# Kernel tuning notes

Measured on AMD Instinct MI355X. Metric: run time of the kernel, lower is better.

## Reference

```python
import jax, jax.numpy as jnp
import numpy as np

S, T, F, J, E, H = 1024, 64, 128, 64, 256, 4
DH = E // H


def layer_norm(x, g, b, eps=1e-10):
    m = jnp.mean(x, axis=-1, keepdims=True)
    v = jnp.mean((x - m) ** 2, axis=-1, keepdims=True)  # population var (correction=0)
    return (x - m) / jnp.sqrt(v + eps) * g + b


def mha(x, Wq, Wk, Wv):
    # x: [B, L, E]; Wq/Wk/Wv: [H, E, DH]. Non-standard: scale AFTER softmax@V.
    q = jnp.einsum('ble,hed->hbld', x, Wq)
    k = jnp.einsum('ble,hed->hbld', x, Wk)
    v = jnp.einsum('ble,hed->hbld', x, Wv)
    w = jax.nn.softmax(jnp.einsum('hbld,hbmd->hblm', q, k), axis=-1)
    o = jnp.einsum('hblm,hbmd->hbld', w, v) / jnp.sqrt(jnp.asarray(Wq.shape[-1], x.dtype))
    h, b, l, d = o.shape
    return jnp.transpose(o, (1, 2, 0, 3)).reshape(b, l, h * d)


def ffn(x, W1, b1, W2, b2):
    return jnp.maximum(x @ W1 + b1, 0.0) @ W2 + b2  # Dropout is identity in eval


def pos_encoding(t, e):
    pos = jnp.arange(t, dtype=jnp.float32)[:, None]
    two_i = jnp.floor(jnp.arange(e, dtype=jnp.float32) / 2.0) * 2.0
    div = jnp.power(jnp.float32(100004.0), two_i / e)
    pe = pos / div  # [t, e]
    pe = pe.at[:, 0::2].set(jnp.sin(pe[:, 0::2]))
    pe = pe.at[:, 1::2].set(jnp.cos(pe[:, 1::2]))
    return pe


def setup_inputs() -> dict:
    key = jax.random.key(0)
    ks = jax.random.split(key, 32)
    s = 0.02
    d = {}
    d['x'] = jax.random.normal(ks[0], (S, T, F + J), dtype=jnp.float32)
    d['gate_W'] = s * jax.random.normal(ks[1], (J, F))
    d['gate_b'] = s * jax.random.normal(ks[2], (F,))
    d['embed_W'] = s * jax.random.normal(ks[3], (F, E))
    d['ln0_g'] = 1.0 + s * jax.random.normal(ks[4], (E,))
    d['ln0_b'] = s * jax.random.normal(ks[5], (E,))
    d['intra_Wq'] = s * jax.random.normal(ks[6], (H, E, DH))
    d['intra_Wk'] = s * jax.random.normal(ks[7], (H, E, DH))
    d['intra_Wv'] = s * jax.random.normal(ks[8], (H, E, DH))
    d['intra_ln_g'] = 1.0 + s * jax.random.normal(ks[9], (E,))
    d['intra_ln_b'] = s * jax.random.normal(ks[10], (E,))
    d['intra_W1'] = s * jax.random.normal(ks[11], (E, 4 * E))
    d['intra_b1'] = s * jax.random.normal(ks[12], (4 * E,))
    d['intra_W2'] = s * jax.random.normal(ks[13], (4 * E, E))
    d['intra_b2'] = s * jax.random.normal(ks[14], (E,))
    d['inter_Wq'] = s * jax.random.normal(ks[15], (H, E, DH))
    d['inter_Wk'] = s * jax.random.normal(ks[16], (H, E, DH))
    d['inter_Wv'] = s * jax.random.normal(ks[17], (H, E, DH))
    d['inter_ln1_g'] = 1.0 + s * jax.random.normal(ks[18], (E,))
    d['inter_ln1_b'] = s * jax.random.normal(ks[19], (E,))
    d['inter_ln2_g'] = 1.0 + s * jax.random.normal(ks[20], (E,))
    d['inter_ln2_b'] = s * jax.random.normal(ks[21], (E,))
    d['inter_W1'] = s * jax.random.normal(ks[22], (E, 4 * E))
    d['inter_b1'] = s * jax.random.normal(ks[23], (4 * E,))
    d['inter_W2'] = s * jax.random.normal(ks[24], (4 * E, E))
    d['inter_b2'] = s * jax.random.normal(ks[25], (E,))
    d['temp_W'] = s * jax.random.normal(ks[26], (E, E))
    d['pred_W'] = s * jax.random.normal(ks[27], (E, 1))
    d['pred_b'] = s * jax.random.normal(ks[28], (1,))
    return d


def reference(x, gate_W, gate_b, embed_W, ln0_g, ln0_b,
              intra_Wq, intra_Wk, intra_Wv, intra_ln_g, intra_ln_b,
              intra_W1, intra_b1, intra_W2, intra_b2,
              inter_Wq, inter_Wk, inter_Wv, inter_ln1_g, inter_ln1_b,
              inter_ln2_g, inter_ln2_b, inter_W1, inter_b1, inter_W2, inter_b2,
              temp_W, pred_W, pred_b):
    # Gating
    x_f = x[..., :F]                       # [S, T, F]
    x_g = x[..., -1, F:]                   # [S, J]
    gate = jax.nn.softmax(x_g @ gate_W + gate_b, axis=-1)[:, None, :]
    x_f = gate * x_f
    # Embed + positional encoding + LN
    emb = x_f @ embed_W                    # [S, T, E]
    res = emb + pos_encoding(T, E)
    ln = layer_norm(res, ln0_g, ln0_b)
    # Intra-stock attention (attend over time axis per stock)
    a = mha(ln, intra_Wq, intra_Wk, intra_Wv)
    r = a + ln
    intra_out = r + ffn(layer_norm(r, intra_ln_g, intra_ln_b), intra_W1, intra_b1, intra_W2, intra_b2)
    # Inter-stock attention (attend over stock axis per timestep)
    xT = jnp.transpose(intra_out, (1, 0, 2))            # [T, S, E]
    xTn = layer_norm(xT, inter_ln1_g, inter_ln1_b)
    a2 = mha(xTn, inter_Wq, inter_Wk, inter_Wv)          # [T, S, E]
    out = jnp.transpose(a2, (1, 0, 2))                   # [S, T, E]
    r2 = out + intra_out
    inter_out = r2 + ffn(layer_norm(r2, inter_ln2_g, inter_ln2_b), inter_W1, inter_b1, inter_W2, inter_b2)
    # Temporal aggregation
    x1 = inter_out @ temp_W                              # [S, T, E]
    cur = x1[..., -1, :][..., :, None]                   # [S, E, 1]
    lam = jax.nn.softmax(jnp.squeeze(x1 @ cur, -1), axis=-1)[:, None, :]  # [S, 1, T]
    agg = jnp.squeeze(lam @ inter_out, -2)               # [S, E]
    # Prediction
    return agg @ pred_W + pred_b                         # [S, 1]
```

## Files before the change

kernel.cpp:

```cpp
#include <hip/hip_runtime.h>


typedef _Float16 h16;
typedef __attribute__((ext_vector_type(8))) _Float16 f16x8;
typedef __attribute__((ext_vector_type(4))) _Float16 f16x4;
typedef __attribute__((ext_vector_type(4))) float f32x4;

__device__ inline float wave_sum(float v){
  #pragma unroll
  for (int o=32;o;o>>=1) v += __shfl_xor(v,o);
  return v;
}
__device__ inline float wave_max(float v){
  #pragma unroll
  for (int o=32;o;o>>=1) v = fmaxf(v,__shfl_xor(v,o));
  return v;
}

__global__ __launch_bounds__(256) void k_pe(float* __restrict__ pe){
  int t = blockIdx.x, i = threadIdx.x;
  float two_i = (float)((i>>1)<<1);
  float dv = powf(100004.0f, two_i*(1.0f/256.0f));
  float v = (float)t / dv;
  pe[t*256+i] = (i&1) ? cosf(v) : sinf(v);
}

__global__ __launch_bounds__(64) void k_gate(const float* __restrict__ x,
    const float* __restrict__ gW, const float* __restrict__ gb,
    float* __restrict__ gate){
  int s = blockIdx.x, lane = threadIdx.x;
  __shared__ float xg[64];
  xg[lane] = x[((size_t)s*64+63)*192 + 128 + lane];
  __syncthreads();
  float a0 = gb[lane], a1 = gb[64+lane];
  #pragma unroll 4
  for (int j=0;j<64;j++){
    float xv = xg[j];
    a0 += xv*gW[j*128+lane];
    a1 += xv*gW[j*128+64+lane];
  }
  float mx = wave_max(fmaxf(a0,a1));
  float e0 = __expf(a0-mx), e1 = __expf(a1-mx);
  float sm = wave_sum(e0+e1);
  gate[s*128+lane]    = e0/sm;
  gate[s*128+64+lane] = e1/sm;
}

__global__ __launch_bounds__(256) void k_t16all(
    const float* __restrict__ q1, const float* __restrict__ k1, const float* __restrict__ v1,
    const float* __restrict__ q2, const float* __restrict__ k2, const float* __restrict__ v2,
    const float* __restrict__ embed_W, const float* __restrict__ temp_W,
    const float* __restrict__ iW1, const float* __restrict__ iW2,
    const float* __restrict__ eW1, const float* __restrict__ eW2,
    h16* __restrict__ base){
  __shared__ float tile[32][33];
  const int b = blockIdx.x, tid = threadIdx.x;
  const float* src; h16* dst; int K, N, tb; bool qkv = false;
  if (b < 384){
    int mat = b>>6; tb = b&63; qkv = true; K = 256; N = 256;
    src = (mat==0)?q1:(mat==1)?k1:(mat==2)?v1:(mat==3)?q2:(mat==4)?k2:v2;
    dst = base + mat*65536;
  } else if (b < 416){ tb = b-384;  K=128;  N=256;  src=embed_W; dst=base+393216; }
  else if (b < 480){ tb = b-416;  K=256;  N=256;  src=temp_W;  dst=base+425984; }
  else if (b < 736){ tb = b-480;  K=256;  N=1024; src=iW1;     dst=base+491520; }
  else if (b < 992){ tb = b-736;  K=1024; N=256;  src=iW2;     dst=base+753664; }
  else if (b < 1248){ tb = b-992; K=256;  N=1024; src=eW1;     dst=base+1015808; }
  else               { tb = b-1248; K=1024; N=256; src=eW2;    dst=base+1277952; }
  const int nt = N>>5;
  const int N0 = (tb & (nt-1))<<5;
  const int K0 = (tb/nt)<<5;
  {
    int r = tid>>3, c0 = (tid&7)<<2;
    int k = K0+r, n = N0+c0;
    const float* p = qkv ? (src + ((n>>6)<<14) + (k<<6) + (n&63))
                         : (src + (size_t)k*N + n);
    float4 v = *(const float4*)p;
    tile[r][c0]=v.x; tile[r][c0+1]=v.y; tile[r][c0+2]=v.z; tile[r][c0+3]=v.w;
  }
  __syncthreads();
  {
    int r = tid>>3, c0 = (tid&7)<<2;
    f16x4 o;
    o[0]=(h16)tile[c0][r]; o[1]=(h16)tile[c0+1][r];
    o[2]=(h16)tile[c0+2][r]; o[3]=(h16)tile[c0+3][r];
    *(f16x4*)(dst + (size_t)(N0+r)*K + K0 + c0) = o;
  }
}

__global__ __launch_bounds__(256) void k_embed(
    const float* __restrict__ x, const h16* __restrict__ Et,
    const float* __restrict__ pe, const float* __restrict__ gate,
    const float* __restrict__ g0, const float* __restrict__ b0,
    float* __restrict__ A){
  __shared__ char pool[65536];
  h16*  As  = (h16*)pool;
  float* res = (float*)pool;
  const int tid = threadIdx.x, lane = tid&63, w = tid>>6;
  const int lr = lane&15, g = lane>>4;
  const int m0 = blockIdx.x<<6;
  #pragma unroll
  for (int it=0; it<8; it++){
    int f4 = it*256 + tid;
    int row = f4>>5, c4 = (f4&31)<<2;
    float4 v = *(const float4*)(x + (size_t)(m0+row)*192 + c4);
    float4 gg = *(const float4*)(gate + (((m0+row)>>6)<<7) + c4);
    v.x*=gg.x; v.y*=gg.y; v.z*=gg.z; v.w*=gg.w;
    int idx = ((row<<7) + c4) ^ ((row&7)<<3);
    f16x4 o; o[0]=(h16)v.x; o[1]=(h16)v.y; o[2]=(h16)v.z; o[3]=(h16)v.w;
    *(f16x4*)&As[idx] = o;
  }
  __syncthreads();
  f32x4 acc[4][4];
  #pragma unroll
  for (int a=0;a<4;a++)
    #pragma unroll
    for (int b=0;b<4;b++) acc[a][b] = (f32x4){0,0,0,0};
  #pragma unroll
  for (int i=0; i<4; i++){
    int kt = (i + w) & 3;
    f16x8 af[4], bf[4];
    #pragma unroll
    for (int rf=0; rf<4; rf++){
      int r = (rf<<4) + lr;
      int idx = ((r<<7) + (kt<<5) + (g<<3)) ^ ((r&7)<<3);
      af[rf] = *(const f16x8*)&As[idx];
    }
    #pragma unroll
    for (int cf=0; cf<4; cf++){
      int n = (w<<6) + (cf<<4) + lr;
      bf[cf] = *(const f16x8*)(Et + (size_t)n*128 + (kt<<5) + (g<<3));
    }
    __builtin_amdgcn_s_setprio(1);
    #pragma unroll
    for (int rf=0; rf<4; rf++)
      #pragma unroll
      for (int cf=0; cf<4; cf++)
        acc[rf][cf] = __builtin_amdgcn_mfma_f32_16x16x32_f16(af[rf], bf[cf], acc[rf][cf], 0,0,0);
    __builtin_amdgcn_s_setprio(0);
  }
  __syncthreads();
  #pragma unroll
  for (int cf=0; cf<4; cf++){
    int col = (w<<6) + (cf<<4) + lr;
    #pragma unroll
    for (int rf=0; rf<4; rf++)
      #pragma unroll
      for (int i=0;i<4;i++){
        int r = (rf<<4) + (g<<2) + i;
        res[(r<<8) + col] = acc[rf][cf][i] + pe[(r<<8) + col];
      }
  }
  __syncthreads();
  {
    float4 gg = *(const float4*)(g0 + (lane<<2));
    float4 bb = *(const float4*)(b0 + (lane<<2));
    for (int rr=0; rr<16; rr++){
      int r = (w<<4) + rr;
      float4 v = *(float4*)&res[(r<<8) + (lane<<2)];
      float sm = wave_sum(v.x+v.y+v.z+v.w);
      float sq = wave_sum(v.x*v.x+v.y*v.y+v.z*v.z+v.w*v.w);
      float mean = sm*(1.f/256.f);
      float rs = rsqrtf(sq*(1.f/256.f) - mean*mean + 1e-10f);
      float4 o;
      o.x=(v.x-mean)*rs*gg.x+bb.x; o.y=(v.y-mean)*rs*gg.y+bb.y;
      o.z=(v.z-mean)*rs*gg.z+bb.z; o.w=(v.w-mean)*rs*gg.w+bb.w;
      *(float4*)(A + (size_t)(m0+r)*256 + (lane<<2)) = o;
    }
  }
}

__global__ __launch_bounds__(512,1) void k_intra(
    const float* __restrict__ A, const h16* __restrict__ Wqkv,
    float* __restrict__ Out){
  __shared__ h16 Xs[64*256];
  __shared__ h16 Qs[4*64*64];
  __shared__ h16 Ks[4*64*64];
  __shared__ h16 VsT[4*64*64];
  __shared__ h16 Ps[8*16*64];
  const int tid = threadIdx.x, lane = tid&63, w = tid>>6;
  const int lr = lane&15, g = lane>>4;
  const int m0 = blockIdx.x<<6;
  #pragma unroll
  for (int rr=0; rr<8; rr++){
    int r = (w<<3) + rr;
    float4 v = *(const float4*)(A + (size_t)(m0+r)*256 + (lane<<2));
    f16x4 o; o[0]=(h16)v.x; o[1]=(h16)v.y; o[2]=(h16)v.z; o[3]=(h16)v.w;
    int idx = ((r<<8) + (lane<<2)) ^ ((r&7)<<3);
    *(f16x4*)&Xs[idx] = o;
  }

  f32x4 aqk[2][2][4];
  f32x4 av[4][2];
  #pragma unroll
  for (int m=0;m<2;m++)
    #pragma unroll
    for (int cf=0;cf<2;cf++)
      #pragma unroll
      for (int mf=0;mf<4;mf++) aqk[m][cf][mf] = (f32x4){0,0,0,0};
  #pragma unroll
  for (int rf=0;rf<4;rf++){ av[rf][0]=(f32x4){0,0,0,0}; av[rf][1]=(f32x4){0,0,0,0}; }

  f16x8 wp[3][2];
  #pragma unroll
  for (int m=0;m<3;m++)
    #pragma unroll
    for (int cf=0;cf<2;cf++){
      int n = (w<<5) + (cf<<4) + lr;
      wp[m][cf] = *(const f16x8*)(Wqkv + (size_t)m*65536 + (size_t)n*256 + (g<<3));
    }
  __syncthreads();

  #pragma unroll
  for (int kt=0; kt<8; kt++){
    f16x8 xf[4], wf[3][2];
    #pragma unroll
    for (int m=0;m<3;m++)
      #pragma unroll
      for (int cf=0;cf<2;cf++) wf[m][cf] = wp[m][cf];
    if (kt<7){
      #pragma unroll
      for (int m=0;m<3;m++)
        #pragma unroll
        for (int cf=0;cf<2;cf++){
          int n = (w<<5) + (cf<<4) + lr;
          wp[m][cf] = *(const f16x8*)(Wqkv + (size_t)m*65536 + (size_t)n*256 + ((kt+1)<<5) + (g<<3));
        }
    }
    #pragma unroll
    for (int rf=0; rf<4; rf++){
      int r = (rf<<4) + lr;
      int idx = ((r<<8) + (kt<<5) + (g<<3)) ^ ((r&7)<<3);
      xf[rf] = *(const f16x8*)&Xs[idx];
    }
    __builtin_amdgcn_s_setprio(1);
    #pragma unroll
    for (int m=0;m<2;m++)
      #pragma unroll
      for (int cf=0;cf<2;cf++)
        #pragma unroll
        for (int mf=0;mf<4;mf++)
          aqk[m][cf][mf] = __builtin_amdgcn_mfma_f32_16x16x32_f16(wf[m][cf], xf[mf], aqk[m][cf][mf], 0,0,0);
    #pragma unroll
    for (int rf=0;rf<4;rf++)
      #pragma unroll
      for (int cf=0;cf<2;cf++)
        av[rf][cf] = __builtin_amdgcn_mfma_f32_16x16x32_f16(xf[rf], wf[2][cf], av[rf][cf], 0,0,0);
    __builtin_amdgcn_s_setprio(0);
  }
  #pragma unroll
  for (int cf=0; cf<2; cf++){
    int n0 = (w<<5) + (cf<<4) + (g<<2);
    int headq = n0>>6, d0 = n0&63;
    int hbq = headq<<12;
    #pragma unroll
    for (int mf=0; mf<4; mf++){
      int q = (mf<<4) + lr;
      int base = (q<<6) + (((d0>>3) ^ (q&7))<<3) + (d0&7);
      f16x4 oq, ok;
      #pragma unroll
      for (int i=0;i<4;i++){ oq[i]=(h16)aqk[0][cf][mf][i]; ok[i]=(h16)aqk[1][cf][mf][i]; }
      *(f16x4*)&Qs[hbq + base] = oq;
      *(f16x4*)&Ks[hbq + base] = ok;
    }
    int nv = (w<<5) + (cf<<4) + lr;
    int headv = nv>>6, dv = nv&63;
    int hbv = headv<<12;
    int vkey = (dv + (dv>>3)) & 7;
    #pragma unroll
    for (int rf=0; rf<4; rf++){
      int q0 = (rf<<4) + (g<<2);
      f16x4 ov;
      #pragma unroll
      for (int i=0;i<4;i++) ov[i]=(h16)av[rf][cf][i];
      *(f16x4*)&VsT[hbv + (dv<<6) + (((q0>>3) ^ vkey)<<3) + (q0&7)] = ov;
    }
  }
  __syncthreads();
  #pragma unroll
  for (int sl=0; sl<2; sl++){
    int slot = w + (sl<<3);
    int head = slot>>2, q0 = (slot&3)<<4;
    const int hb = head<<12;
    f16x8 qf[2];
    #pragma unroll
    for (int ks=0; ks<2; ks++)
      qf[ks] = *(const f16x8*)&Qs[hb + ((q0+lr)<<6) + (((g + (ks<<2)) ^ (lr&7))<<3)];
    f32x4 sa[4];
    #pragma unroll
    for (int mm=0;mm<4;mm++) sa[mm] = (f32x4){0,0,0,0};
    __builtin_amdgcn_s_setprio(1);
    #pragma unroll
    for (int ks=0; ks<2; ks++)
      #pragma unroll
      for (int mm=0;mm<4;mm++){
        int krow = (mm<<4) + lr;
        f16x8 af = *(const f16x8*)&Ks[hb + (krow<<6) + (((g + (ks<<2)) ^ (krow&7))<<3)];
        sa[mm] = __builtin_amdgcn_mfma_f32_16x16x32_f16(af, qf[ks], sa[mm], 0,0,0);
      }
    __builtin_amdgcn_s_setprio(0);
    float pmax = -1e30f;
    #pragma unroll
    for (int mm=0;mm<4;mm++)
      #pragma unroll
      for (int i=0;i<4;i++) pmax = fmaxf(pmax, sa[mm][i]);
    pmax = fmaxf(pmax, __shfl_xor(pmax, 16));
    pmax = fmaxf(pmax, __shfl_xor(pmax, 32));
    float ps = 0.f;
    f16x4 pv[4];
    #pragma unroll
    for (int mm=0;mm<4;mm++)
      #pragma unroll
      for (int i=0;i<4;i++){
        float p = __expf(sa[mm][i] - pmax);
        ps += p;
        pv[mm][i] = (h16)p;
      }
    ps += __shfl_xor(ps, 16);
    ps += __shfl_xor(ps, 32);
    const int pbase = w<<10;
    #pragma unroll
    for (int mm=0;mm<4;mm++){
      int k0 = (mm<<4) + (g<<2);
      int unit = k0>>3, off = k0&7;
      *(f16x4*)&Ps[pbase + (lr<<6) + ((unit ^ (lr&7))<<3) + off] = pv[mm];
    }
    f32x4 oc[4];
    #pragma unroll
    for (int cf=0;cf<4;cf++) oc[cf] = (f32x4){0,0,0,0};
    __builtin_amdgcn_s_setprio(1);
    #pragma unroll
    for (int ks=0; ks<2; ks++){
      f16x8 pa = *(const f16x8*)&Ps[pbase + (lr<<6) + (((g + (ks<<2)) ^ (lr&7))<<3)];
      #pragma unroll
      for (int cf=0;cf<4;cf++){
        int d = (cf<<4) + lr;
        int key = (d + (d>>3)) & 7;
        f16x8 bf = *(const f16x8*)&VsT[hb + (d<<6) + (((g + (ks<<2)) ^ key)<<3)];
        oc[cf] = __builtin_amdgcn_mfma_f32_16x16x32_f16(pa, bf, oc[cf], 0,0,0);
      }
    }
    __builtin_amdgcn_s_setprio(0);
    float linv = 1.0f/(ps*8.0f);
    #pragma unroll
    for (int i=0;i<4;i++){
      float li = __shfl(linv, (g<<4) + (g<<2) + i);
      int row = m0 + q0 + (g<<2) + i;
      #pragma unroll
      for (int cf=0;cf<4;cf++){
        int col = (head<<6) + (cf<<4) + lr;
        size_t ga = (size_t)row*256 + col;
        Out[ga] = oc[cf][i]*li + A[ga];
      }
    }
  }
}

__global__ __launch_bounds__(512) void k_qkv4(
    const float* __restrict__ X,
    const float* __restrict__ lng, const float* __restrict__ lnb,
    const h16* __restrict__ Bt0,
    h16* __restrict__ Qh, h16* __restrict__ Kh, h16* __restrict__ Vh){
  __shared__ h16 Xs[64*256];
  const int tid = threadIdx.x, lane = tid&63, w = tid>>6;
  const int lr = lane&15, g = lane>>4;
  const int m0 = blockIdx.x<<6;
  {
    float4 gg = *(const float4*)(lng + (lane<<2));
    float4 bb = *(const float4*)(lnb + (lane<<2));
    #pragma unroll
    for (int rr=0; rr<8; rr++){
      int r = (w<<3) + rr;
      float4 v = *(const float4*)(X + (size_t)(m0+r)*256 + (lane<<2));
      float sm = wave_sum(v.x+v.y+v.z+v.w);
      float sq = wave_sum(v.x*v.x+v.y*v.y+v.z*v.z+v.w*v.w);
      float mean = sm*(1.f/256.f);
      float rs = rsqrtf(sq*(1.f/256.f) - mean*mean + 1e-10f);
      v.x=(v.x-mean)*rs*gg.x+bb.x; v.y=(v.y-mean)*rs*gg.y+bb.y;
      v.z=(v.z-mean)*rs*gg.z+bb.z; v.w=(v.w-mean)*rs*gg.w+bb.w;
      f16x4 o; o[0]=(h16)v.x; o[1]=(h16)v.y; o[2]=(h16)v.z; o[3]=(h16)v.w;
      int idx = ((r<<8) + (lane<<2)) ^ ((r&7)<<3);
      *(f16x4*)&Xs[idx] = o;
    }
  }
  f32x4 acc[3][2][4];
  #pragma unroll
  for (int m=0;m<3;m++)
    #pragma unroll
    for (int cf=0;cf<2;cf++)
      #pragma unroll
      for (int mf=0;mf<4;mf++) acc[m][cf][mf] = (f32x4){0,0,0,0};
  f16x8 wp[3][2];
  #pragma unroll
  for (int m=0;m<3;m++)
    #pragma unroll
    for (int cf=0;cf<2;cf++){
      int n = (w<<5) + (cf<<4) + lr;
      wp[m][cf] = *(const f16x8*)(Bt0 + (size_t)m*65536 + (size_t)n*256 + ((w&7)<<5) + (g<<3));
    }
  __syncthreads();
  #pragma unroll
  for (int i=0; i<8; i++){
    int kt = (i + w) & 7;
    f16x8 xf[4], wfr[3][2];
    #pragma unroll
    for (int m=0;m<3;m++)
      #pragma unroll
      for (int cf=0;cf<2;cf++) wfr[m][cf] = wp[m][cf];
    if (i<7){
      int ktn = (i + 1 + w) & 7;
      #pragma unroll
      for (int m=0;m<3;m++)
        #pragma unroll
        for (int cf=0;cf<2;cf++){
          int n = (w<<5) + (cf<<4) + lr;
          wp[m][cf] = *(const f16x8*)(Bt0 + (size_t)m*65536 + (size_t)n*256 + (ktn<<5) + (g<<3));
        }
    }
    #pragma unroll
    for (int mf=0; mf<4; mf++){
      int r = (mf<<4) + lr;
      int idx = ((r<<8) + (kt<<5) + (g<<3)) ^ ((r&7)<<3);
      xf[mf] = *(const f16x8*)&Xs[idx];
    }
    __builtin_amdgcn_s_setprio(1);
    #pragma unroll
    for (int m=0;m<3;m++)
      #pragma unroll
      for (int cf=0;cf<2;cf++)
        #pragma unroll
        for (int mf=0;mf<4;mf++)
          acc[m][cf][mf] = __builtin_amdgcn_mfma_f32_16x16x32_f16(wfr[m][cf], xf[mf], acc[m][cf][mf], 0,0,0);
    __builtin_amdgcn_s_setprio(0);
  }
  #pragma unroll
  for (int m=0;m<3;m++){
    h16* dst = (m==0)?Qh:(m==1)?Kh:Vh;
    #pragma unroll
    for (int cf=0;cf<2;cf++){
      int n0 = (w<<5) + (cf<<4) + (g<<2);
      #pragma unroll
      for (int mf=0; mf<4; mf++){
        int row = m0 + (mf<<4) + lr;
        f16x4 o;
        #pragma unroll
        for (int i=0;i<4;i++) o[i] = (h16)acc[m][cf][mf][i];
        *(f16x4*)(dst + (size_t)row*256 + n0) = o;
      }
    }
  }
}

template<int NT, int QG>
__global__ __launch_bounds__(256) void k_attn16(
    const h16* __restrict__ Qh, const h16* __restrict__ Kh, const h16* __restrict__ Vh,
    const float* __restrict__ Resid, float* __restrict__ Out){
  __shared__ h16 Ks[64*64];
  __shared__ h16 VsT[64*64];
  __shared__ h16 Ps[4*QG*16*64];
  const int tid = threadIdx.x, lane = tid&63, w = tid>>6;
  const int lr = lane&15, g = lane>>4;
  const int hh = blockIdx.x, t = blockIdx.y, qc = blockIdx.z;
  const int ccol = hh<<6;

  f16x8 qf[QG][2];
  #pragma unroll
  for (int grp=0; grp<QG; grp++){
    int ql = grp*64 + (w<<4) + lr;
    size_t m = ((size_t)qc*(64*QG) + ql)*64 + t;
    const h16* qp = Qh + m*256 + ccol + (g<<3);
    qf[grp][0] = *(const f16x8*)qp;
    qf[grp][1] = *(const f16x8*)(qp + 32);
  }

  f32x4 oc[QG][4];
  float m_r[QG], l_r[QG];
  #pragma unroll
  for (int grp=0; grp<QG; grp++){
    #pragma unroll
    for (int cf=0;cf<4;cf++) oc[grp][cf] = (f32x4){0,0,0,0};
    m_r[grp] = -1e30f; l_r[grp] = 0.f;
  }

  for (int kb=0; kb<NT; kb++){
    __syncthreads();
    #pragma unroll
    for (int it=0; it<2; it++){
      int u = it*256 + tid;
      int row = u>>3, un = u&7;
      size_t m = ((size_t)kb*64 + row)*64 + t;
      f16x8 kv = *(const f16x8*)(Kh + m*256 + ccol + (un<<3));
      *(f16x8*)&Ks[(row<<6) + ((un ^ (row&7))<<3)] = kv;
      f16x8 vv = *(const f16x8*)(Vh + m*256 + ccol + (un<<3));
      #pragma unroll
      for (int j=0;j<8;j++){
        int d = (un<<3) + j;
        int key = (d + un) & 7;
        VsT[(d<<6) + ((((row>>3) ^ key))<<3) + (row&7)] = vv[j];
      }
    }
    __syncthreads();
    #pragma unroll
    for (int grp=0; grp<QG; grp++){
      f32x4 sa[4];
      #pragma unroll
      for (int mm=0;mm<4;mm++) sa[mm] = (f32x4){0,0,0,0};
      __builtin_amdgcn_s_setprio(1);
      #pragma unroll
      for (int ks=0; ks<2; ks++){
        #pragma unroll
        for (int mm=0;mm<4;mm++){
          int krow = (mm<<4) + lr;
          f16x8 af = *(const f16x8*)&Ks[(krow<<6) + (((g + (ks<<2)) ^ (krow&7))<<3)];
          sa[mm] = __builtin_amdgcn_mfma_f32_16x16x32_f16(af, qf[grp][ks], sa[mm], 0,0,0);
        }
      }
      __builtin_amdgcn_s_setprio(0);
      float pmax = -1e30f;
      #pragma unroll
      for (int mm=0;mm<4;mm++)
        #pragma unroll
        for (int i=0;i<4;i++) pmax = fmaxf(pmax, sa[mm][i]);
      pmax = fmaxf(pmax, __shfl_xor(pmax, 16));
      pmax = fmaxf(pmax, __shfl_xor(pmax, 32));
      float mn = fmaxf(m_r[grp], pmax);
      float sca = __expf(m_r[grp] - mn);
      m_r[grp] = mn;
      float ps = 0.f;
      f16x4 pv[4];
      #pragma unroll
      for (int mm=0;mm<4;mm++){
        #pragma unroll
        for (int i=0;i<4;i++){
          float p = __expf(sa[mm][i] - mn);
          ps += p;
          pv[mm][i] = (h16)p;
        }
      }
      ps += __shfl_xor(ps, 16);
      ps += __shfl_xor(ps, 32);
      l_r[grp] = l_r[grp]*sca + ps;
      const int pbase = ((w*QG + grp)<<10);
      #pragma unroll
      for (int mm=0;mm<4;mm++){
        int k0 = (mm<<4) + (g<<2);
        int unit = k0>>3, off = k0&7;
        *(f16x4*)&Ps[pbase + (lr<<6) + ((unit ^ (lr&7))<<3) + off] = pv[mm];
      }
      #pragma unroll
      for (int i=0;i<4;i++){
        float si = __shfl(sca, (g<<4) + (g<<2) + i);
        #pragma unroll
        for (int cf=0;cf<4;cf++) oc[grp][cf][i] *= si;
      }
      __builtin_amdgcn_s_setprio(1);
      #pragma unroll
      for (int ks=0; ks<2; ks++){
        f16x8 pa = *(const f16x8*)&Ps[pbase + (lr<<6) + (((g + (ks<<2)) ^ (lr&7))<<3)];
        #pragma unroll
        for (int cf=0;cf<4;cf++){
          int d = (cf<<4) + lr;
          int key = (d + (d>>3)) & 7;
          f16x8 bf = *(const f16x8*)&VsT[(d<<6) + (((g + (ks<<2)) ^ key)<<3)];
          oc[grp][cf] = __builtin_amdgcn_mfma_f32_16x16x32_f16(pa, bf, oc[grp][cf], 0,0,0);
        }
      }
      __builtin_amdgcn_s_setprio(0);
    }
  }
  #pragma unroll
  for (int grp=0; grp<QG; grp++){
    float linv = 1.0f/(l_r[grp]*8.0f);
    #pragma unroll
    for (int i=0;i<4;i++){
      float li = __shfl(linv, (g<<4) + (g<<2) + i);
      int ql = grp*64 + (w<<4) + (g<<2) + i;
      size_t m = ((size_t)qc*(64*QG) + ql)*64 + t;
      #pragma unroll
      for (int cf=0;cf<4;cf++){
        int d = (cf<<4) + lr;
        size_t ga = m*256 + ccol + d;
        Out[ga] = oc[grp][cf][i]*li + Resid[ga];
      }
    }
  }
}

__global__ __launch_bounds__(512,1) void k_ffn5(
    const float* X, float* Out,
    const float* __restrict__ lng, const float* __restrict__ lnb,
    const h16* __restrict__ W1t, const float* __restrict__ b1,
    const h16* __restrict__ W2t, const float* __restrict__ b2){
  __shared__ h16 Xs[64*256];
  __shared__ h16 Hc[64*1024];
  const int tid  = threadIdx.x;
  const int lane = tid & 63;
  const int w    = tid >> 6;
  const int r0   = blockIdx.x << 6;
  const int lr   = lane & 15;
  const int g    = lane >> 4;
  {
    float4 gg = *(const float4*)(lng + (lane<<2));
    float4 bb = *(const float4*)(lnb + (lane<<2));
    #pragma unroll
    for (int rr=0; rr<8; rr++){
      int r = (w<<3) + rr;
      float4 v = *(const float4*)(X + (size_t)(r0+r)*256 + (lane<<2));
      float sm = wave_sum(v.x+v.y+v.z+v.w);
      float sq = wave_sum(v.x*v.x+v.y*v.y+v.z*v.z+v.w*v.w);
      float mean = sm*(1.f/256.f);
      float rs = rsqrtf(sq*(1.f/256.f) - mean*mean + 1e-10f);
      f16x4 o;
      o[0]=(h16)((v.x-mean)*rs*gg.x+bb.x); o[1]=(h16)((v.y-mean)*rs*gg.y+bb.y);
      o[2]=(h16)((v.z-mean)*rs*gg.z+bb.z); o[3]=(h16)((v.w-mean)*rs*gg.w+bb.w);
      int idx = ((r<<8) + (lane<<2)) ^ ((r&7)<<3);
      *(f16x4*)&Xs[idx] = o;
    }
  }
  {
    f32x4 acc1[8][4];
    #pragma unroll
    for (int a=0;a<8;a++)
      #pragma unroll
      for (int b=0;b<4;b++) acc1[a][b] = (f32x4){0,0,0,0};
    f16x8 wp[8];
    #pragma unroll
    for (int nf=0; nf<8; nf++){
      int n = (w<<7) + (nf<<4) + lr;
      wp[nf] = *(const f16x8*)(W1t + (size_t)n*256 + ((w&7)<<5) + (g<<3));
    }
    __syncthreads();
    #pragma unroll
    for (int i=0; i<8; i++){
      int kt = (i + w) & 7;
      f16x8 xf[4], wfr[8];
      #pragma unroll
      for (int nf=0; nf<8; nf++) wfr[nf] = wp[nf];
      if (i<7){
        int ktn = (i + 1 + w) & 7;
        #pragma unroll
        for (int nf=0; nf<8; nf++){
          int n = (w<<7) + (nf<<4) + lr;
          wp[nf] = *(const f16x8*)(W1t + (size_t)n*256 + (ktn<<5) + (g<<3));
        }
      }
      #pragma unroll
      for (int mf=0; mf<4; mf++){
        int r = (mf<<4) + lr;
        int idx = ((r<<8) + (kt<<5) + (g<<3)) ^ ((r&7)<<3);
        xf[mf] = *(const f16x8*)&Xs[idx];
      }
      __builtin_amdgcn_s_setprio(1);
      #pragma unroll
      for (int nf=0; nf<8; nf++)
        #pragma unroll
        for (int mf=0; mf<4; mf++)
          acc1[nf][mf] = __builtin_amdgcn_mfma_f32_16x16x32_f16(
              wfr[nf], xf[mf], acc1[nf][mf], 0, 0, 0);
      __builtin_amdgcn_s_setprio(0);
    }
    #pragma unroll
    for (int nf=0; nf<8; nf++){
      int n0 = (w<<7) + (nf<<4) + (g<<2);
      float4 bq = *(const float4*)(b1 + n0);
      #pragma unroll
      for (int mf=0; mf<4; mf++){
        int m = (mf<<4) + lr;
        f16x4 o;
        o[0]=(h16)fmaxf(acc1[nf][mf][0]+bq.x,0.f);
        o[1]=(h16)fmaxf(acc1[nf][mf][1]+bq.y,0.f);
        o[2]=(h16)fmaxf(acc1[nf][mf][2]+bq.z,0.f);
        o[3]=(h16)fmaxf(acc1[nf][mf][3]+bq.w,0.f);
        *(f16x4*)&Hc[((m<<10) + n0) ^ ((m&7)<<3)] = o;
      }
    }
  }
  __syncthreads();
  f32x4 acc2[4][2];
  #pragma unroll
  for (int a=0;a<4;a++){ acc2[a][0]=(f32x4){0,0,0,0}; acc2[a][1]=(f32x4){0,0,0,0}; }
  f16x8 wp2[2][2];
  #pragma unroll
  for (int s=0;s<2;s++){
    int kt = (s + (w<<2)) & 31;
    #pragma unroll
    for (int cf=0;cf<2;cf++){
      int n = (w<<5) + (cf<<4) + lr;
      wp2[s][cf] = *(const f16x8*)(W2t + (size_t)n*1024 + (kt<<5) + (g<<3));
    }
  }
  #pragma unroll
  for (int i=0; i<32; i++){
    const int sl = i&1;
    int kt = (i + (w<<2)) & 31;
    f16x8 af[4], bf[2];
    bf[0] = wp2[sl][0]; bf[1] = wp2[sl][1];
    if (i<30){
      int ktn = ((i+2) + (w<<2)) & 31;
      #pragma unroll
      for (int cf=0;cf<2;cf++){
        int n = (w<<5) + (cf<<4) + lr;
        wp2[sl][cf] = *(const f16x8*)(W2t + (size_t)n*1024 + (ktn<<5) + (g<<3));
      }
    }
    #pragma unroll
    for (int rf=0; rf<4; rf++){
      int r = (rf<<4) + lr;
      int idx = ((r<<10) + (kt<<5) + (g<<3)) ^ ((r&7)<<3);
      af[rf] = *(const f16x8*)&Hc[idx];
    }
    __builtin_amdgcn_s_setprio(1);
    #pragma unroll
    for (int rf=0; rf<4; rf++)
      #pragma unroll
      for (int cf=0; cf<2; cf++)
        acc2[rf][cf] = __builtin_amdgcn_mfma_f32_16x16x32_f16(
            af[rf], bf[cf], acc2[rf][cf], 0, 0, 0);
    __builtin_amdgcn_s_setprio(0);
  }
  #pragma unroll
  for (int cf=0; cf<2; cf++){
    int col = (w<<5) + (cf<<4) + lr;
    float bv = b2[col];
    #pragma unroll
    for (int rf=0; rf<4; rf++){
      #pragma unroll
      for (int i=0;i<4;i++){
        size_t r = (size_t)r0 + (rf<<4) + (g<<2) + i;
        float res = X[r*256 + col];
        Out[r*256 + col] = acc2[rf][cf][i] + bv + res;
      }
    }
  }
}

__global__ __launch_bounds__(256) void k_head(
    const float* __restrict__ Bb, const h16* __restrict__ Tt,
    const float* __restrict__ predW, const float* __restrict__ predb,
    float* __restrict__ out){
  __shared__ h16 Xs[64*256];
  __shared__ float X1s[64*256];
  __shared__ float lam[64];
  __shared__ float red[4];
  const int tid = threadIdx.x, lane = tid&63, w = tid>>6;
  const int lr = lane&15, g = lane>>4;
  const size_t m0 = (size_t)blockIdx.x<<6;
  #pragma unroll
  for (int it=0; it<16; it++){
    int f4 = it*256 + tid;
    int row = f4>>6, c4 = (f4&63)<<2;
    float4 v = *(const float4*)(Bb + (m0+row)*256 + c4);
    int idx = ((row<<8) + c4) ^ ((row&7)<<3);
    f16x4 o; o[0]=(h16)v.x; o[1]=(h16)v.y; o[2]=(h16)v.z; o[3]=(h16)v.w;
    *(f16x4*)&Xs[idx] = o;
  }
  __syncthreads();
  f32x4 acc[4][4];
  #pragma unroll
  for (int rf=0;rf<4;rf++)
    #pragma unroll
    for (int cf=0;cf<4;cf++) acc[rf][cf] = (f32x4){0,0,0,0};
  #pragma unroll
  for (int kt=0; kt<8; kt++){
    f16x8 af[4], bf[4];
    #pragma unroll
    for (int rf=0; rf<4; rf++){
      int r = (rf<<4) + lr;
      int idx = ((r<<8) + (kt<<5) + (g<<3)) ^ ((r&7)<<3);
      af[rf] = *(const f16x8*)&Xs[idx];
    }
    #pragma unroll
    for (int cf=0; cf<4; cf++){
      int n = (w<<6) + (cf<<4) + lr;
      bf[cf] = *(const f16x8*)(Tt + (size_t)n*256 + (kt<<5) + (g<<3));
    }
    __builtin_amdgcn_s_setprio(1);
    #pragma unroll
    for (int rf=0; rf<4; rf++)
      #pragma unroll
      for (int cf=0; cf<4; cf++)
        acc[rf][cf] = __builtin_amdgcn_mfma_f32_16x16x32_f16(af[rf], bf[cf], acc[rf][cf], 0,0,0);
    __builtin_amdgcn_s_setprio(0);
  }
  #pragma unroll
  for (int cf=0; cf<4; cf++){
    int col = (w<<6) + (cf<<4) + lr;
    #pragma unroll
    for (int rf=0; rf<4; rf++)
      #pragma unroll
      for (int i=0;i<4;i++){
        int r = (rf<<4) + (g<<2) + i;
        X1s[(r<<8) + col] = acc[rf][cf][i];
      }
  }
  __syncthreads();
  float lg[16];
  for (int r=0;r<16;r++){
    int trow = (w<<4) + r;
    float4 xa = *(float4*)&X1s[(trow<<8) + (lane<<2)];
    float4 xc = *(float4*)&X1s[(63<<8) + (lane<<2)];
    lg[r] = wave_sum(xa.x*xc.x + xa.y*xc.y + xa.z*xc.z + xa.w*xc.w);
  }
  if (lane==0){
    #pragma unroll
    for (int r=0;r<16;r++) lam[(w<<4)+r] = lg[r];
  }
  __syncthreads();
  if (tid < 64){
    float v = lam[tid];
    float mx = wave_max(v);
    float p = __expf(v-mx);
    float sm = wave_sum(p);
    lam[tid] = p/sm;
  }
  __syncthreads();
  float ag = 0.f;
  for (int t=0;t<64;t++)
    ag += lam[t]*(float)Xs[((t<<8)+tid) ^ ((t&7)<<3)];
  float wsum = wave_sum(ag * predW[tid]);
  if (lane==0) red[w] = wsum;
  __syncthreads();
  if (tid==0) out[blockIdx.x] = red[0]+red[1]+red[2]+red[3] + predb[0];
}

extern "C" void kernel_launch(void* const* d_in, const int* in_sizes, int n_in,
                              void* d_out, int out_size, void* d_ws, size_t ws_size,
                              hipStream_t stream){
  const float* x       = (const float*)d_in[0];
  const float* gate_W  = (const float*)d_in[1];
  const float* gate_b  = (const float*)d_in[2];
  const float* embed_W = (const float*)d_in[3];
  const float* ln0_g   = (const float*)d_in[4];
  const float* ln0_b   = (const float*)d_in[5];
  const float* iln_g   = (const float*)d_in[9];
  const float* iln_b   = (const float*)d_in[10];
  const float* iW1     = (const float*)d_in[11];
  const float* ib1     = (const float*)d_in[12];
  const float* iW2     = (const float*)d_in[13];
  const float* ib2     = (const float*)d_in[14];
  const float* eln1_g  = (const float*)d_in[18];
  const float* eln1_b  = (const float*)d_in[19];
  const float* eln2_g  = (const float*)d_in[20];
  const float* eln2_b  = (const float*)d_in[21];
  const float* eW1     = (const float*)d_in[22];
  const float* eb1     = (const float*)d_in[23];
  const float* eW2     = (const float*)d_in[24];
  const float* eb2     = (const float*)d_in[25];
  const float* temp_W  = (const float*)d_in[26];
  const float* pred_W  = (const float*)d_in[27];
  const float* pred_b  = (const float*)d_in[28];
  float* out = (float*)d_out;

  float* pe    = (float*)d_ws;
  float* gate  = pe + 16384;
  h16* fQKV = (h16*)((char*)d_ws + ((size_t)4<<20));
  h16* fE   = fQKV + 393216;
  h16* fT   = fE + 32768;
  h16* fW1i = fT + 65536;
  h16* fW2i = fW1i + 262144;
  h16* fW1e = fW2i + 262144;
  h16* fW2e = fW1e + 262144;
  const size_t MR = (size_t)65536*256;
  float* A  = (float*)((char*)d_ws + ((size_t)8<<20));
  float* Bb = A + MR;
  h16* Qh2 = (h16*)A;
  h16* Kh2 = Qh2 + MR;
  h16* Vh2 = (h16*)(Bb + MR);

  k_pe  <<<64,  256, 0, stream>>>(pe);
  k_gate<<<1024, 64, 0, stream>>>(x, gate_W, gate_b, gate);
  k_t16all<<<1504,256,0,stream>>>(
      (const float*)d_in[6],(const float*)d_in[7],(const float*)d_in[8],
      (const float*)d_in[15],(const float*)d_in[16],(const float*)d_in[17],
      embed_W, temp_W, iW1, iW2, eW1, eW2, fQKV);

  k_embed<<<1024,256,0,stream>>>(x, fE, pe, gate, ln0_g, ln0_b, A);

  k_intra<<<1024,512,0,stream>>>(A, fQKV, Bb);
  k_ffn5<<<1024,512,0,stream>>>(Bb, Bb, iln_g, iln_b, fW1i, ib1, fW2i, ib2);

  k_qkv4<<<1024,512,0,stream>>>(Bb, eln1_g, eln1_b, fQKV + 3*65536, Qh2, Kh2, Vh2);
  k_attn16<16,1><<<dim3(4,64,16),256,0,stream>>>(Qh2, Kh2, Vh2, Bb, Bb);
  k_ffn5<<<1024,512,0,stream>>>(Bb, Bb, eln2_g, eln2_b, fW1e, eb1, fW2e, eb2);

  k_head<<<1024,256,0,stream>>>(Bb, fT, pred_W, pred_b, out);
}
```

Measured before the change: 719.9 us.

## Split fused FFN into layernorm kernel plus tiled global_load_lds GEMMs

The fused per-64-row FFN kernel is replaced by three stages: a standalone layernorm kernel that writes fp16 activations, a 128x128-tiled GEMM that writes a ReLU'd fp16 hidden buffer to global memory, and a second GEMM that adds bias and residual. The GEMMs stage tiles with global_load_lds and run in four chunks of 16384 rows so the hidden buffer fits in the workspace. The aim is better weight reuse and occupancy than the single-block fused kernel. The cost is extra global traffic for the hidden activations, more kernel launches, and no double buffering in the K loop.

```diff
diff --git a/kernel.cpp b/kernel.cpp
--- a/kernel.cpp
+++ b/kernel.cpp
@@ -5,6 +5,13 @@
 typedef __attribute__((ext_vector_type(8))) _Float16 f16x8;
 typedef __attribute__((ext_vector_type(4))) _Float16 f16x4;
 typedef __attribute__((ext_vector_type(4))) float f32x4;
+
+__device__ __forceinline__ void gl16(const h16* g, h16* l){
+  __builtin_amdgcn_global_load_lds(
+    (const __attribute__((address_space(1))) unsigned int*)g,
+    (__attribute__((address_space(3))) unsigned int*)l,
+    16, 0, 0);
+}
 
 __device__ inline float wave_sum(float v){
   #pragma unroll
@@ -585,150 +592,109 @@
   }
 }
 
-__global__ __launch_bounds__(512,1) void k_ffn5(
-    const float* X, float* Out,
-    const float* __restrict__ lng, const float* __restrict__ lnb,
-    const h16* __restrict__ W1t, const float* __restrict__ b1,
-    const h16* __restrict__ W2t, const float* __restrict__ b2){
-  __shared__ h16 Xs[64*256];
-  __shared__ h16 Hc[64*1024];
-  const int tid  = threadIdx.x;
-  const int lane = tid & 63;
-  const int w    = tid >> 6;
-  const int r0   = blockIdx.x << 6;
-  const int lr   = lane & 15;
-  const int g    = lane >> 4;
-  {
-    float4 gg = *(const float4*)(lng + (lane<<2));
-    float4 bb = *(const float4*)(lnb + (lane<<2));
-    #pragma unroll
-    for (int rr=0; rr<8; rr++){
-      int r = (w<<3) + rr;
-      float4 v = *(const float4*)(X + (size_t)(r0+r)*256 + (lane<<2));
-      float sm = wave_sum(v.x+v.y+v.z+v.w);
-      float sq = wave_sum(v.x*v.x+v.y*v.y+v.z*v.z+v.w*v.w);
-      float mean = sm*(1.f/256.f);
-      float rs = rsqrtf(sq*(1.f/256.f) - mean*mean + 1e-10f);
-      f16x4 o;
-      o[0]=(h16)((v.x-mean)*rs*gg.x+bb.x); o[1]=(h16)((v.y-mean)*rs*gg.y+bb.y);
-      o[2]=(h16)((v.z-mean)*rs*gg.z+bb.z); o[3]=(h16)((v.w-mean)*rs*gg.w+bb.w);
-      int idx = ((r<<8) + (lane<<2)) ^ ((r&7)<<3);
-      *(f16x4*)&Xs[idx] = o;
-    }
-  }
-  {
-    f32x4 acc1[8][4];
-    #pragma unroll
-    for (int a=0;a<8;a++)
-      #pragma unroll
-      for (int b=0;b<4;b++) acc1[a][b] = (f32x4){0,0,0,0};
-    f16x8 wp[8];
-    #pragma unroll
-    for (int nf=0; nf<8; nf++){
-      int n = (w<<7) + (nf<<4) + lr;
-      wp[nf] = *(const f16x8*)(W1t + (size_t)n*256 + ((w&7)<<5) + (g<<3));
+__global__ __launch_bounds__(256) void k_lnh(const float* __restrict__ in,
+    const float* __restrict__ g, const float* __restrict__ b,
+    h16* __restrict__ out){
+  const int wv = threadIdx.x>>6, lane = threadIdx.x&63;
+  const size_t row = (size_t)blockIdx.x*4 + wv;
+  float4 v = *(const float4*)(in + row*256 + (lane<<2));
+  float sm = wave_sum(v.x+v.y+v.z+v.w);
+  float sq = wave_sum(v.x*v.x+v.y*v.y+v.z*v.z+v.w*v.w);
+  float mean = sm*(1.f/256.f);
+  float rs = rsqrtf(sq*(1.f/256.f) - mean*mean + 1e-10f);
+  float4 gg = *(const float4*)(g + (lane<<2));
+  float4 bb = *(const float4*)(b + (lane<<2));
+  f16x4 o;
+  o[0]=(h16)((v.x-mean)*rs*gg.x+bb.x); o[1]=(h16)((v.y-mean)*rs*gg.y+bb.y);
+  o[2]=(h16)((v.z-mean)*rs*gg.z+bb.z); o[3]=(h16)((v.w-mean)*rs*gg.w+bb.w);
+  *(f16x4*)(out + row*256 + (lane<<2)) = o;
+}
+
+template<int KDIM, int MODE>
+__global__ __launch_bounds__(256,2) void k_gemm97(
+    const h16* __restrict__ Am,
+    const h16* __restrict__ Bt,
+    const float* __restrict__ bias,
+    const float* __restrict__ Resid,
+    void* __restrict__ Cv){
+  __shared__ h16 As[128*32];
+  __shared__ h16 Bs[128*32];
+  const int tid = threadIdx.x, lane = tid&63, w = tid>>6;
+  const int lr = lane&15, g = lane>>4;
+  const int m0 = blockIdx.x<<7, n0 = blockIdx.y<<7;
+  const int wr = w>>1, wc = w&1;
+  f32x4 acc[4][4];
+  #pragma unroll
+  for (int a=0;a<4;a++)
+    #pragma unroll
+    for (int b=0;b<4;b++) acc[a][b] = (f32x4){0,0,0,0};
+
+  for (int kt=0; kt<KDIM/32; kt++){
+    #pragma unroll
+    for (int j=0;j<2;j++){
+      int row = (j<<6) + (tid>>2);
+      int un  = tid&3;
+      gl16(Am + (size_t)(m0+row)*KDIM + (kt<<5) + (un<<3),
+           &As[(((j<<8)+(w<<6))<<3)]);
+      gl16(Bt + (size_t)(n0+row)*KDIM + (kt<<5) + (un<<3),
+           &Bs[(((j<<8)+(w<<6))<<3)]);
     }
     __syncthreads();
-    #pragma unroll
-    for (int i=0; i<8; i++){
-      int kt = (i + w) & 7;
-      f16x8 xf[4], wfr[8];
-      #pragma unroll
-      for (int nf=0; nf<8; nf++) wfr[nf] = wp[nf];
-      if (i<7){
-        int ktn = (i + 1 + w) & 7;
-        #pragma unroll
-        for (int nf=0; nf<8; nf++){
-          int n = (w<<7) + (nf<<4) + lr;
-          wp[nf] = *(const f16x8*)(W1t + (size_t)n*256 + (ktn<<5) + (g<<3));
+    f16x8 af[4], bf[4];
+    #pragma unroll
+    for (int rf=0;rf<4;rf++)
+      af[rf] = *(const f16x8*)&As[((wr<<6)+(rf<<4)+lr)*32 + (g<<3)];
+    #pragma unroll
+    for (int cf=0;cf<4;cf++)
+      bf[cf] = *(const f16x8*)&Bs[((wc<<6)+(cf<<4)+lr)*32 + (g<<3)];
+    __builtin_amdgcn_s_setprio(1);
+    if (MODE==1){
+      #pragma unroll
+      for (int cf=0;cf<4;cf++)
+        #pragma unroll
+        for (int rf=0;rf<4;rf++)
+          acc[cf][rf] = __builtin_amdgcn_mfma_f32_16x16x32_f16(bf[cf], af[rf], acc[cf][rf], 0,0,0);
+    } else {
+      #pragma unroll
+      for (int rf=0;rf<4;rf++)
+        #pragma unroll
+        for (int cf=0;cf<4;cf++)
+          acc[rf][cf] = __builtin_amdgcn_mfma_f32_16x16x32_f16(af[rf], bf[cf], acc[rf][cf], 0,0,0);
+    }
+    __builtin_amdgcn_s_setprio(0);
+    __syncthreads();
+  }
+
+  if (MODE==1){
+    h16* Hm = (h16*)Cv;
+    #pragma unroll
+    for (int cf=0;cf<4;cf++){
+      int nb = n0 + (wc<<6) + (cf<<4) + (g<<2);
+      float4 bq = *(const float4*)(bias + nb);
+      #pragma unroll
+      for (int rf=0;rf<4;rf++){
+        int m = m0 + (wr<<6) + (rf<<4) + lr;
+        f16x4 o;
+        o[0]=(h16)fmaxf(acc[cf][rf][0]+bq.x,0.f);
+        o[1]=(h16)fmaxf(acc[cf][rf][1]+bq.y,0.f);
+        o[2]=(h16)fmaxf(acc[cf][rf][2]+bq.z,0.f);
+        o[3]=(h16)fmaxf(acc[cf][rf][3]+bq.w,0.f);
+        *(f16x4*)&Hm[(size_t)m*1024 + nb] = o;
+      }
+    }
+  } else {
+    float* O = (float*)Cv;
+    #pragma unroll
+    for (int cf=0;cf<4;cf++){
+      int n = n0 + (wc<<6) + (cf<<4) + lr;
+      float bv = bias[n];
+      #pragma unroll
+      for (int rf=0;rf<4;rf++)
+        #pragma unroll
+        for (int i=0;i<4;i++){
+          size_t m = (size_t)m0 + (wr<<6) + (rf<<4) + (g<<2) + i;
+          O[m*256 + n] = acc[rf][cf][i] + bv + Resid[m*256 + n];
         }
-      }
-      #pragma unroll
-      for (int mf=0; mf<4; mf++){
-        int r = (mf<<4) + lr;
-        int idx = ((r<<8) + (kt<<5) + (g<<3)) ^ ((r&7)<<3);
-        xf[mf] = *(const f16x8*)&Xs[idx];
-      }
-      __builtin_amdgcn_s_setprio(1);
-      #pragma unroll
-      for (int nf=0; nf<8; nf++)
-        #pragma unroll
-        for (int mf=0; mf<4; mf++)
-          acc1[nf][mf] = __builtin_amdgcn_mfma_f32_16x16x32_f16(
-              wfr[nf], xf[mf], acc1[nf][mf], 0, 0, 0);
-      __builtin_amdgcn_s_setprio(0);
-    }
-    #pragma unroll
-    for (int nf=0; nf<8; nf++){
-      int n0 = (w<<7) + (nf<<4) + (g<<2);
-      float4 bq = *(const float4*)(b1 + n0);
-      #pragma unroll
-      for (int mf=0; mf<4; mf++){
-        int m = (mf<<4) + lr;
-        f16x4 o;
-        o[0]=(h16)fmaxf(acc1[nf][mf][0]+bq.x,0.f);
-        o[1]=(h16)fmaxf(acc1[nf][mf][1]+bq.y,0.f);
-        o[2]=(h16)fmaxf(acc1[nf][mf][2]+bq.z,0.f);
-        o[3]=(h16)fmaxf(acc1[nf][mf][3]+bq.w,0.f);
-        *(f16x4*)&Hc[((m<<10) + n0) ^ ((m&7)<<3)] = o;
-      }
-    }
-  }
-  __syncthreads();
-  f32x4 acc2[4][2];
-  #pragma unroll
-  for (int a=0;a<4;a++){ acc2[a][0]=(f32x4){0,0,0,0}; acc2[a][1]=(f32x4){0,0,0,0}; }
-  f16x8 wp2[2][2];
-  #pragma unroll
-  for (int s=0;s<2;s++){
-    int kt = (s + (w<<2)) & 31;
-    #pragma unroll
-    for (int cf=0;cf<2;cf++){
-      int n = (w<<5) + (cf<<4) + lr;
-      wp2[s][cf] = *(const f16x8*)(W2t + (size_t)n*1024 + (kt<<5) + (g<<3));
-    }
-  }
-  #pragma unroll
-  for (int i=0; i<32; i++){
-    const int sl = i&1;
-    int kt = (i + (w<<2)) & 31;
-    f16x8 af[4], bf[2];
-    bf[0] = wp2[sl][0]; bf[1] = wp2[sl][1];
-    if (i<30){
-      int ktn = ((i+2) + (w<<2)) & 31;
-      #pragma unroll
-      for (int cf=0;cf<2;cf++){
-        int n = (w<<5) + (cf<<4) + lr;
-        wp2[sl][cf] = *(const f16x8*)(W2t + (size_t)n*1024 + (ktn<<5) + (g<<3));
-      }
-    }
-    #pragma unroll
-    for (int rf=0; rf<4; rf++){
-      int r = (rf<<4) + lr;
-      int idx = ((r<<10) + (kt<<5) + (g<<3)) ^ ((r&7)<<3);
-      af[rf] = *(const f16x8*)&Hc[idx];
-    }
-    __builtin_amdgcn_s_setprio(1);
-    #pragma unroll
-    for (int rf=0; rf<4; rf++)
-      #pragma unroll
-      for (int cf=0; cf<2; cf++)
-        acc2[rf][cf] = __builtin_amdgcn_mfma_f32_16x16x32_f16(
-            af[rf], bf[cf], acc2[rf][cf], 0, 0, 0);
-    __builtin_amdgcn_s_setprio(0);
-  }
-  #pragma unroll
-  for (int cf=0; cf<2; cf++){
-    int col = (w<<5) + (cf<<4) + lr;
-    float bv = b2[col];
-    #pragma unroll
-    for (int rf=0; rf<4; rf++){
-      #pragma unroll
-      for (int i=0;i<4;i++){
-        size_t r = (size_t)r0 + (rf<<4) + (g<<2) + i;
-        float res = X[r*256 + col];
-        Out[r*256 + col] = acc2[rf][cf][i] + bv + res;
-      }
     }
   }
 }
@@ -862,6 +828,8 @@
   const size_t MR = (size_t)65536*256;
   float* A  = (float*)((char*)d_ws + ((size_t)8<<20));
   float* Bb = A + MR;
+  h16* Xh  = (h16*)A;
+  h16* Hq  = (h16*)(Bb + MR);
   h16* Qh2 = (h16*)A;
   h16* Kh2 = Qh2 + MR;
   h16* Vh2 = (h16*)(Bb + MR);
@@ -876,11 +844,23 @@
   k_embed<<<1024,256,0,stream>>>(x, fE, pe, gate, ln0_g, ln0_b, A);
 
   k_intra<<<1024,512,0,stream>>>(A, fQKV, Bb);
-  k_ffn5<<<1024,512,0,stream>>>(Bb, Bb, iln_g, iln_b, fW1i, ib1, fW2i, ib2);
+
+  k_lnh<<<16384,256,0,stream>>>(Bb, iln_g, iln_b, Xh);
+  for (int q=0; q<4; q++){
+    const size_t mo = (size_t)q*16384;
+    k_gemm97<256,1><<<dim3(128,8),256,0,stream>>>(Xh + mo*256, fW1i, ib1, nullptr, Hq);
+    k_gemm97<1024,2><<<dim3(128,2),256,0,stream>>>(Hq, fW2i, ib2, Bb + mo*256, Bb + mo*256);
+  }
 
   k_qkv4<<<1024,512,0,stream>>>(Bb, eln1_g, eln1_b, fQKV + 3*65536, Qh2, Kh2, Vh2);
   k_attn16<16,1><<<dim3(4,64,16),256,0,stream>>>(Qh2, Kh2, Vh2, Bb, Bb);
-  k_ffn5<<<1024,512,0,stream>>>(Bb, Bb, eln2_g, eln2_b, fW1e, eb1, fW2e, eb2);
+
+  k_lnh<<<16384,256,0,stream>>>(Bb, eln2_g, eln2_b, Xh);
+  for (int q=0; q<4; q++){
+    const size_t mo = (size_t)q*16384;
+    k_gemm97<256,1><<<dim3(128,8),256,0,stream>>>(Xh + mo*256, fW1e, eb1, nullptr, Hq);
+    k_gemm97<1024,2><<<dim3(128,2),256,0,stream>>>(Hq, fW2e, eb2, Bb + mo*256, Bb + mo*256);
+  }
 
   k_head<<<1024,256,0,stream>>>(Bb, fT, pred_W, pred_b, out);
 }
```

Result: slower. 789.7 us (+9.7%).
